# Optimization experiments

Measured on AMD Instinct MI355X. Metric: run time of the kernel, lower is better.

Reference implementation:

```python
import jax, jax.numpy as jnp
import numpy as np

B, T, H = 64, 1024, 256

def _lstm_cell(x, h, c, Wih, Whh, bih, bhh):
    # torch gate order: i, f, g, o
    gates = x @ Wih.T + h @ Whh.T + bih + bhh  # [B, 4H]
    i, f, g, o = jnp.split(gates, 4, axis=-1)
    i = jax.nn.sigmoid(i)
    f = jax.nn.sigmoid(f)
    g = jnp.tanh(g)
    o = jax.nn.sigmoid(o)
    c_new = f * c + i * g
    h_new = o * jnp.tanh(c_new)
    return h_new, c_new


def setup_inputs() -> dict:
    key = jax.random.key(0)
    ks = jax.random.split(key, 11)
    s = 1.0 / np.sqrt(H)
    def u(k, shape):
        return jax.random.uniform(k, shape, jnp.float32, -s, s)
    return {
        "x": jax.random.normal(ks[0], (B, T, 1), jnp.float32),
        "enc_Wih": u(ks[1], (4 * H, 1)),
        "enc_Whh": u(ks[2], (4 * H, H)),
        "enc_bih": u(ks[3], (4 * H,)),
        "enc_bhh": u(ks[4], (4 * H,)),
        "dec_Wih": u(ks[5], (4 * H, 1)),
        "dec_Whh": u(ks[6], (4 * H, H)),
        "dec_bih": u(ks[7], (4 * H,)),
        "dec_bhh": u(ks[8], (4 * H,)),
        "lin_W": u(ks[9], (1, 2 * H)),
        "lin_b": u(ks[10], (1,)),
    }


def reference(x, enc_Wih, enc_Whh, enc_bih, enc_bhh,
              dec_Wih, dec_Whh, dec_bih, dec_bhh, lin_W, lin_b):
    b = x.shape[0]
    h = x.shape[2] * 0  # placeholder, not used
    hidden = enc_Whh.shape[1]

    x_t = jnp.transpose(x, (1, 0, 2))  # [T, B, 1]

    # ---- encoder: single-layer LSTM over time ----
    def enc_step(carry, xt):
        hh, cc = carry
        hh, cc = _lstm_cell(xt, hh, cc, enc_Wih, enc_Whh, enc_bih, enc_bhh)
        return (hh, cc), hh
    h0 = jnp.zeros((b, hidden), x.dtype)
    (h_last, _), enc_seq = jax.lax.scan(enc_step, (h0, h0), x_t)
    encoder_states = jnp.transpose(enc_seq, (1, 0, 2))  # [B, T, H]

    # ---- decoder: LSTMCell + dot attention + linear, per step ----
    def dec_step(carry, xt):
        hx, cx = carry
        hx, cx = _lstm_cell(xt, hx, cx, dec_Wih, dec_Whh, dec_bih, dec_bhh)
        scores = jnp.einsum('bth,bh->bt', encoder_states, hx)  # dot attention
        attn = jax.nn.softmax(scores, axis=1)
        ctx = jnp.einsum('bt,bth->bh', attn, encoder_states)
        updated = jnp.concatenate([ctx, hx], axis=1)  # [B, 2H]
        res = updated @ lin_W.T + lin_b  # [B, 1]
        return (hx, cx), res

    cx0 = jnp.zeros_like(h_last)
    _, outs = jax.lax.scan(dec_step, (h_last, cx0), x_t)  # [T, B, 1]
    return jnp.transpose(outs, (1, 0, 2))  # [B, T, 1]
```

## Files before the change

### kernel.cpp

```cpp
#include <hip/hip_runtime.h>
#include <math.h>

#define HD 256
#define GD 1024
#define TT 1024
#define BB 64
#define NT 512

typedef float __attribute__((ext_vector_type(4))) f32x4;

__device__ __forceinline__ float sig_(float x)  { return 1.f / (1.f + __expf(-x)); }
__device__ __forceinline__ float tanh_(float x) { return 1.f - 2.f / (1.f + __expf(2.f * x)); }

__global__ __launch_bounds__(256) void prep_kernel(
    const float* __restrict__ eW, const float* __restrict__ eb1, const float* __restrict__ eb2,
    const float* __restrict__ dW, const float* __restrict__ db1, const float* __restrict__ db2,
    float* __restrict__ WTe, float* __restrict__ WTd,
    float* __restrict__ be, float* __restrict__ bd,
    unsigned long long* __restrict__ ex,
    unsigned* __restrict__ prog4)
{
    int idx = blockIdx.x * 256 + threadIdx.x;
    if (idx < GD * HD) {
        int j = idx / HD, k = idx % HD;
        WTe[k * GD + j] = eW[idx];
        WTd[k * GD + j] = dW[idx];
    }
    if (idx < GD) {
        be[idx] = eb1[idx] + eb2[idx];
        bd[idx] = db1[idx] + db2[idx];
    }
    if (idx < BB * 2 * 256) ex[idx] = 0ULL;
    if (idx < BB * 4) prog4[idx] = 0u;
}

__device__ __forceinline__ void scan_body(
    const float* __restrict__ x, const float* __restrict__ Wih,
    const float* __restrict__ bias, const float* __restrict__ WT,
    const float* __restrict__ h_init, float* __restrict__ states,
    unsigned long long* __restrict__ ex, unsigned tag0,
    const float* __restrict__ lw, float* __restrict__ qdot,
    unsigned* __restrict__ prog4,
    float* x_s, float* h_rep , float* act_s ,
    int b, int q)
{
    const int tid = threadIdx.x;
    const int s   = tid & 3;
    const int jj  = tid >> 2;
    const int gate = jj >> 5;
    const int kk0  = (jj & 31) * 2;
    const int r0   = gate * 64 + kk0;
    const int jg0  = gate * 256 + q * 64 + kk0;

    float4 w0[16], w1[16];
    {
        const float* basek = WT + (size_t)(s * 64) * GD;
        #pragma unroll
        for (int i = 0; i < 16; ++i) {
            const float* p0 = basek + (size_t)(4 * i) * GD + jg0;
            w0[i] = make_float4(p0[0], p0[GD], p0[2 * GD], p0[3 * GD]);
            const float* p1 = p0 + 1;
            w1[i] = make_float4(p1[0], p1[GD], p1[2 * GD], p1[3 * GD]);
        }
    }
    const float wih0 = Wih[jg0], wih1 = Wih[jg0 + 1];
    const float bj0  = bias[jg0], bj1  = bias[jg0 + 1];
    const float lwd  = lw ? lw[tid & 255] : 0.f;

    for (int i = tid; i < TT; i += NT) x_s[i] = x[b * TT + i];
    if (tid < 256) {
        float hv = h_init ? h_init[((size_t)b * TT + (TT - 1)) * HD + tid] : 0.f;
        h_rep[(tid >> 6) * 264 + (tid & 63)] = hv;
    }
    float c = 0.f;
    __syncthreads();

    #pragma unroll 1
    for (int t = 0; t < TT; ++t) {
        __builtin_amdgcn_s_setprio(1);
        const float xt = x_s[t];
        float a0p, a1p, a0q = 0.f, a1q = 0.f;
        if (s == 0) { a0p = fmaf(xt, wih0, bj0); a1p = fmaf(xt, wih1, bj1); }
        else        { a0p = 0.f;                 a1p = 0.f; }
        const float4* h4 = (const float4*)(h_rep + s * 264);
        #pragma unroll
        for (int i = 0; i < 8; ++i) {
            float4 hv = h4[i];
            a0p = fmaf(hv.x, w0[i].x, a0p); a0p = fmaf(hv.y, w0[i].y, a0p);
            a0p = fmaf(hv.z, w0[i].z, a0p); a0p = fmaf(hv.w, w0[i].w, a0p);
            a1p = fmaf(hv.x, w1[i].x, a1p); a1p = fmaf(hv.y, w1[i].y, a1p);
            a1p = fmaf(hv.z, w1[i].z, a1p); a1p = fmaf(hv.w, w1[i].w, a1p);
        }
        #pragma unroll
        for (int i = 8; i < 16; ++i) {
            float4 hv = h4[i];
            a0q = fmaf(hv.x, w0[i].x, a0q); a0q = fmaf(hv.y, w0[i].y, a0q);
            a0q = fmaf(hv.z, w0[i].z, a0q); a0q = fmaf(hv.w, w0[i].w, a0q);
            a1q = fmaf(hv.x, w1[i].x, a1q); a1q = fmaf(hv.y, w1[i].y, a1q);
            a1q = fmaf(hv.z, w1[i].z, a1q); a1q = fmaf(hv.w, w1[i].w, a1q);
        }
        float a0 = a0p + a0q;
        float a1 = a1p + a1q;
        a0 += __shfl_xor(a0, 1); a0 += __shfl_xor(a0, 2);
        a1 += __shfl_xor(a1, 1); a1 += __shfl_xor(a1, 2);
        if (s == 0) {
            float2 av;
            av.x = (gate == 2) ? tanh_(a0) : sig_(a0);
            av.y = (gate == 2) ? tanh_(a1) : sig_(a1);
            *(float2*)(&act_s[r0]) = av;
        }
        __syncthreads();

        const unsigned tag = tag0 + (unsigned)t + 1u;
        unsigned long long* ssl = ex + ((size_t)b * 2 + (t & 1)) * 256;
        if (tid < 256) {
            const int dq = tid >> 6, dk = tid & 63;
            if (dq == q) {
                float gi = act_s[dk], gf = act_s[64 + dk], gg = act_s[128 + dk], go = act_s[192 + dk];
                c = fmaf(gf, c, gi * gg);
                float h = go * tanh_(c);
                unsigned long long pk = ((unsigned long long)tag << 32)
                                      | (unsigned long long)__float_as_uint(h);
                __hip_atomic_store(&ssl[tid], pk, __ATOMIC_RELAXED, __HIP_MEMORY_SCOPE_AGENT);
                h_rep[q * 264 + dk] = h;
                float* sp = &states[((size_t)(b * TT + t)) * HD + tid];
                asm volatile("global_store_dword %0, %1, off sc0 sc1"
                             :: "v"(sp), "v"(h) : "memory");
                __builtin_amdgcn_s_setprio(0);
                if (lw) {
                    float v = h * lwd;
                    #pragma unroll
                    for (int m = 1; m < 64; m <<= 1) v += __shfl_xor(v, m);
                    if (dk == 0) qdot[((size_t)(b * TT + t)) * 4 + q] = v;
                }
            } else {
                __builtin_amdgcn_s_setprio(0);
                unsigned long long u;
                const unsigned long long* sp = ssl + tid;
                do {
                    u = __hip_atomic_load(sp, __ATOMIC_RELAXED, __HIP_MEMORY_SCOPE_AGENT);
                } while ((unsigned)(u >> 32) != tag);
                h_rep[dq * 264 + dk] = __uint_as_float((unsigned)u);
            }
        } else {
            __builtin_amdgcn_s_setprio(0);
        }
        __syncthreads();
        if (prog4 && ((t & 31) == 31) && tid == 0)
            __hip_atomic_store(&prog4[b * 4 + q], (unsigned)((t + 1) >> 5),
                               __ATOMIC_RELAXED, __HIP_MEMORY_SCOPE_AGENT);
    }
}

__global__ __launch_bounds__(NT, 2) void enc_kernel(
    const float* __restrict__ x, const float* __restrict__ Wih,
    const float* __restrict__ bias, const float* __restrict__ WT,
    float* __restrict__ states, unsigned long long* __restrict__ ex,
    const float* __restrict__ lw, float* __restrict__ qew)
{
    __shared__ float x_s[TT];
    __shared__ float h_rep[4 * 264];
    __shared__ float act_s[256];
    const int b = (int)blockIdx.x & 63;
    const int q = (int)blockIdx.x >> 6;
    scan_body(x, Wih, bias, WT, nullptr, states, ex, 0u, lw, qew, nullptr,
              x_s, h_rep, act_s, b, q);
}

#define SMEMF 17440
__global__ __launch_bounds__(NT, 2) void tail_kernel(
    const float* __restrict__ x, const float* __restrict__ Wih,
    const float* __restrict__ bias, const float* __restrict__ WT,
    const float* __restrict__ enc_states, float* __restrict__ dec_hs,
    unsigned long long* __restrict__ ex,
    unsigned* __restrict__ prog4,
    const float* __restrict__ qew, const float* __restrict__ lw2,
    const float* __restrict__ lin_b, float* __restrict__ out)
{
    __shared__ __align__(16) float smem[SMEMF];
    const int blk = (int)blockIdx.x;
    const int tid = threadIdx.x;

    if (blk < 256) {
        float* x_s   = smem;
        float* h_rep = smem + 1024;
        float* act_s = smem + 1024 + 4 * 264;
        scan_body(x, Wih, bias, WT, enc_states, dec_hs, ex, 1024u,
                  nullptr, nullptr, prog4, x_s, h_rep, act_s, blk & 63, blk >> 6);
        return;
    }

    const int ai   = blk - 256;
    const int b    = ai & 63;
    const int tile = ai >> 6;
    const int td0  = tile * 32;
    float* Hx   = smem;
    float* E    = smem + 9216;
    float* hw_s = smem + 17408;

    if (tid == 0) {
        const unsigned need = (unsigned)tile + 1u;
        for (;;) {
            unsigned m0 = __hip_atomic_load(&prog4[b*4+0], __ATOMIC_RELAXED, __HIP_MEMORY_SCOPE_AGENT);
            unsigned m1 = __hip_atomic_load(&prog4[b*4+1], __ATOMIC_RELAXED, __HIP_MEMORY_SCOPE_AGENT);
            unsigned m2 = __hip_atomic_load(&prog4[b*4+2], __ATOMIC_RELAXED, __HIP_MEMORY_SCOPE_AGENT);
            unsigned m3 = __hip_atomic_load(&prog4[b*4+3], __ATOMIC_RELAXED, __HIP_MEMORY_SCOPE_AGENT);
            unsigned mn = min(min(m0, m1), min(m2, m3));
            if (mn >= need) break;
            __builtin_amdgcn_s_sleep(8);
        }
        (void)__hip_atomic_load(&prog4[b*4], __ATOMIC_ACQUIRE, __HIP_MEMORY_SCOPE_AGENT);
    }
    __syncthreads();

    {
        const int td = tid >> 4;
        const int kq = tid & 15;
        const int kc = kq * 16;
        const float* src = dec_hs + ((size_t)b * TT + td0 + td) * HD + kc;
        f32x4 v0, v1, v2, v3;
        asm volatile(
            "global_load_dwordx4 %0, %4, off sc0 sc1\n\t"
            "global_load_dwordx4 %1, %5, off sc0 sc1\n\t"
            "global_load_dwordx4 %2, %6, off sc0 sc1\n\t"
            "global_load_dwordx4 %3, %7, off sc0 sc1\n\t"
            "s_waitcnt vmcnt(0)"
            : "=&v"(v0), "=&v"(v1), "=&v"(v2), "=&v"(v3)
            : "v"(src), "v"(src + 4), "v"(src + 8), "v"(src + 12)
            : "memory");
        const float4 w20 = ((const float4*)(lw2 + kc))[0];
        const float4 w21 = ((const float4*)(lw2 + kc))[1];
        const float4 w22 = ((const float4*)(lw2 + kc))[2];
        const float4 w23 = ((const float4*)(lw2 + kc))[3];
        float ph = 0.f;
        Hx[(kc+ 0)*36+td]=v0.x; Hx[(kc+ 1)*36+td]=v0.y; Hx[(kc+ 2)*36+td]=v0.z; Hx[(kc+ 3)*36+td]=v0.w;
        Hx[(kc+ 4)*36+td]=v1.x; Hx[(kc+ 5)*36+td]=v1.y; Hx[(kc+ 6)*36+td]=v1.z; Hx[(kc+ 7)*36+td]=v1.w;
        Hx[(kc+ 8)*36+td]=v2.x; Hx[(kc+ 9)*36+td]=v2.y; Hx[(kc+10)*36+td]=v2.z; Hx[(kc+11)*36+td]=v2.w;
        Hx[(kc+12)*36+td]=v3.x; Hx[(kc+13)*36+td]=v3.y; Hx[(kc+14)*36+td]=v3.z; Hx[(kc+15)*36+td]=v3.w;
        ph = fmaf(v0.x, w20.x, ph); ph = fmaf(v0.y, w20.y, ph);
        ph = fmaf(v0.z, w20.z, ph); ph = fmaf(v0.w, w20.w, ph);
        ph = fmaf(v1.x, w21.x, ph); ph = fmaf(v1.y, w21.y, ph);
        ph = fmaf(v1.z, w21.z, ph); ph = fmaf(v1.w, w21.w, ph);
        ph = fmaf(v2.x, w22.x, ph); ph = fmaf(v2.y, w22.y, ph);
        ph = fmaf(v2.z, w22.z, ph); ph = fmaf(v2.w, w22.w, ph);
        ph = fmaf(v3.x, w23.x, ph); ph = fmaf(v3.y, w23.y, ph);
        ph = fmaf(v3.z, w23.z, ph); ph = fmaf(v3.w, w23.w, ph);
        E[td * 16 + kq] = ph;
    }
    __syncthreads();
    if (tid < 32) {
        float sum = 0.f;
        #pragma unroll
        for (int j = 0; j < 16; ++j) sum += E[tid * 16 + j];
        hw_s[tid] = sum;
    }

    const int tdt = tid >> 5;
    const int tet = tid & 31;

    float M[2]  = {-1e30f, -1e30f};
    float Nm[2] = {0.f, 0.f};
    float Dn[2] = {0.f, 0.f};

    for (int tc = 0; tc < 4; ++tc) {
        const int te0 = tc * 256;
        float S[2][8] = {{0.f}};
        for (int kc8 = 0; kc8 < 8; ++kc8) {
            const int k0 = kc8 * 32;
            __syncthreads();
            {
                const int te = tid & 255, half = tid >> 8;
                const float* src = enc_states + ((size_t)b * TT + te0 + te) * HD + k0 + half * 16;
                #pragma unroll
                for (int j = 0; j < 4; ++j) {
                    float4 v = ((const float4*)src)[j];
                    E[(half * 16 + j * 4 + 0) * 256 + te] = v.x;
                    E[(half * 16 + j * 4 + 1) * 256 + te] = v.y;
                    E[(half * 16 + j * 4 + 2) * 256 + te] = v.z;
                    E[(half * 16 + j * 4 + 3) * 256 + te] = v.w;
                }
            }
            __syncthreads();
            #pragma unroll 8
            for (int k = 0; k < 32; ++k) {
                const float2 hx2 = *(const float2*)(&Hx[(k0 + k) * 36 + tdt * 2]);
                #pragma unroll
                for (int i = 0; i < 8; ++i) {
                    const float e = E[k * 256 + tet + 32 * i];
                    S[0][i] = fmaf(hx2.x, e, S[0][i]);
                    S[1][i] = fmaf(hx2.y, e, S[1][i]);
                }
            }
        }
        float ewv[8];
        #pragma unroll
        for (int i = 0; i < 8; ++i) {
            const float4 e4 = ((const float4*)qew)[(size_t)b * TT + te0 + tet + 32 * i];
            ewv[i] = (e4.x + e4.y) + (e4.z + e4.w);
        }
        #pragma unroll
        for (int r = 0; r < 2; ++r) {
            float cm = S[r][0];
            #pragma unroll
            for (int i = 1; i < 8; ++i) cm = fmaxf(cm, S[r][i]);
            #pragma unroll
            for (int m = 1; m < 32; m <<= 1) cm = fmaxf(cm, __shfl_xor(cm, m));
            const float newM  = fmaxf(M[r], cm);
            const float scale = __expf(M[r] - newM);
            float nl = 0.f, dl = 0.f;
            #pragma unroll
            for (int i = 0; i < 8; ++i) {
                const float p = __expf(S[r][i] - newM);
                dl += p;
                nl = fmaf(p, ewv[i], nl);
            }
            #pragma unroll
            for (int m = 1; m < 32; m <<= 1) {
                nl += __shfl_xor(nl, m);
                dl += __shfl_xor(dl, m);
            }
            Nm[r] = Nm[r] * scale + nl;
            Dn[r] = Dn[r] * scale + dl;
            M[r]  = newM;
        }
    }

    if (tet == 0) {
        const float lb = lin_b[0];
        #pragma unroll
        for (int r = 0; r < 2; ++r) {
            const int row = tdt * 2 + r;
            out[(size_t)b * TT + td0 + row] = Nm[r] / Dn[r] + hw_s[row] + lb;
        }
    }
}

extern "C" void kernel_launch(void* const* d_in, const int* in_sizes, int n_in,
                              void* d_out, int out_size, void* d_ws, size_t ws_size,
                              hipStream_t stream)
{
    const float* x    = (const float*)d_in[0];
    const float* eWih = (const float*)d_in[1];
    const float* eWhh = (const float*)d_in[2];
    const float* ebih = (const float*)d_in[3];
    const float* ebhh = (const float*)d_in[4];
    const float* dWih = (const float*)d_in[5];
    const float* dWhh = (const float*)d_in[6];
    const float* dbih = (const float*)d_in[7];
    const float* dbhh = (const float*)d_in[8];
    const float* linW = (const float*)d_in[9];
    const float* linb = (const float*)d_in[10];
    float* out = (float*)d_out;

    float* p = (float*)d_ws;
    float* WTe = p;        p += (size_t)GD * HD;
    float* WTd = p;        p += (size_t)GD * HD;
    float* be  = p;        p += GD;
    float* bd  = p;        p += GD;
    float* enc_states = p; p += (size_t)BB * TT * HD;
    float* dec_hs = p;     p += (size_t)BB * TT * HD;
    float* qew = p;        p += (size_t)BB * TT * 4;
    unsigned long long* ex = (unsigned long long*)p; p += (size_t)BB * 2 * 256 * 2;
    unsigned* prog4 = (unsigned*)p; p += 256;

    prep_kernel<<<(GD * HD + 255) / 256, 256, 0, stream>>>(
        eWhh, ebih, ebhh, dWhh, dbih, dbhh, WTe, WTd, be, bd, ex, prog4);

    enc_kernel<<<256, NT, 0, stream>>>(
        x, eWih, be, WTe, enc_states, ex, linW, qew);

    tail_kernel<<<256 + BB * (TT / 32), NT, 0, stream>>>(
        x, dWih, bd, WTd, enc_states, dec_hs, ex, prog4,
        qew, linW + HD, linb, out);
}
```

Measured before the change: 4.336 ms.

## Double attention tile to 64 decoder rows and compute hx·lin_W inside scan

The attention blocks now each handle 64 decoder timesteps, with 4 rows per thread instead of 2. This halves the number of attention blocks and the number of times each block re-reads the encoder states, at the cost of more registers and shared memory per block. The decoder scan now computes the per-quarter hx·lin_W dot product itself and writes it to a new buffer, so the attention blocks no longer have to compute it. The setprio raise is also hoisted out of the time loop, which keeps the scan blocks at high priority for the whole loop.

Result: faster. 3.997 ms (-7.8%).

```diff
diff --git a/kernel.cpp b/kernel.cpp
--- a/kernel.cpp
+++ b/kernel.cpp
@@ -39,7 +39,7 @@
     const float* __restrict__ bias, const float* __restrict__ WT,
     const float* __restrict__ h_init, float* __restrict__ states,
     unsigned long long* __restrict__ ex, unsigned tag0,
-    const float* __restrict__ lw, float* __restrict__ qdot,
+    const float* __restrict__ lw, float* __restrict__ qdot, int wt,
     unsigned* __restrict__ prog4,
     float* x_s, float* h_rep , float* act_s ,
     int b, int q)
@@ -75,9 +75,9 @@
     float c = 0.f;
     __syncthreads();
 
+    __builtin_amdgcn_s_setprio(1);
     #pragma unroll 1
     for (int t = 0; t < TT; ++t) {
-        __builtin_amdgcn_s_setprio(1);
         const float xt = x_s[t];
         float a0p, a1p, a0q = 0.f, a1q = 0.f;
         if (s == 0) { a0p = fmaf(xt, wih0, bj0); a1p = fmaf(xt, wih1, bj1); }
@@ -126,15 +126,21 @@
                 float* sp = &states[((size_t)(b * TT + t)) * HD + tid];
                 asm volatile("global_store_dword %0, %1, off sc0 sc1"
                              :: "v"(sp), "v"(h) : "memory");
-                __builtin_amdgcn_s_setprio(0);
                 if (lw) {
                     float v = h * lwd;
                     #pragma unroll
                     for (int m = 1; m < 64; m <<= 1) v += __shfl_xor(v, m);
-                    if (dk == 0) qdot[((size_t)(b * TT + t)) * 4 + q] = v;
+                    if (dk == 0) {
+                        float* qp = &qdot[((size_t)(b * TT + t)) * 4 + q];
+                        if (wt) {
+                            asm volatile("global_store_dword %0, %1, off sc0 sc1"
+                                         :: "v"(qp), "v"(v) : "memory");
+                        } else {
+                            *qp = v;
+                        }
+                    }
                 }
             } else {
-                __builtin_amdgcn_s_setprio(0);
                 unsigned long long u;
                 const unsigned long long* sp = ssl + tid;
                 do {
@@ -142,14 +148,13 @@
                 } while ((unsigned)(u >> 32) != tag);
                 h_rep[dq * 264 + dk] = __uint_as_float((unsigned)u);
             }
-        } else {
-            __builtin_amdgcn_s_setprio(0);
         }
         __syncthreads();
         if (prog4 && ((t & 31) == 31) && tid == 0)
             __hip_atomic_store(&prog4[b * 4 + q], (unsigned)((t + 1) >> 5),
                                __ATOMIC_RELAXED, __HIP_MEMORY_SCOPE_AGENT);
     }
+    __builtin_amdgcn_s_setprio(0);
 }
 
 __global__ __launch_bounds__(NT, 2) void enc_kernel(
@@ -163,18 +168,20 @@
     __shared__ float act_s[256];
     const int b = (int)blockIdx.x & 63;
     const int q = (int)blockIdx.x >> 6;
-    scan_body(x, Wih, bias, WT, nullptr, states, ex, 0u, lw, qew, nullptr,
+    scan_body(x, Wih, bias, WT, nullptr, states, ex, 0u, lw, qew, 0, nullptr,
               x_s, h_rep, act_s, b, q);
 }
 
-#define SMEMF 17440
+#define SMEMF 18752
+#define TDA   64
 __global__ __launch_bounds__(NT, 2) void tail_kernel(
     const float* __restrict__ x, const float* __restrict__ Wih,
     const float* __restrict__ bias, const float* __restrict__ WT,
     const float* __restrict__ enc_states, float* __restrict__ dec_hs,
     unsigned long long* __restrict__ ex,
     unsigned* __restrict__ prog4,
-    const float* __restrict__ qew, const float* __restrict__ lw2,
+    const float* __restrict__ qew, float* __restrict__ qhw,
+    const float* __restrict__ lw2,
     const float* __restrict__ lin_b, float* __restrict__ out)
 {
     __shared__ __align__(16) float smem[SMEMF];
@@ -186,20 +193,20 @@
         float* h_rep = smem + 1024;
         float* act_s = smem + 1024 + 4 * 264;
         scan_body(x, Wih, bias, WT, enc_states, dec_hs, ex, 1024u,
-                  nullptr, nullptr, prog4, x_s, h_rep, act_s, blk & 63, blk >> 6);
+                  lw2, qhw, 1, prog4, x_s, h_rep, act_s, blk & 63, blk >> 6);
         return;
     }
 
     const int ai   = blk - 256;
     const int b    = ai & 63;
     const int tile = ai >> 6;
-    const int td0  = tile * 32;
+    const int td0  = tile * TDA;
     float* Hx   = smem;
-    float* E    = smem + 9216;
-    float* hw_s = smem + 17408;
+    float* E    = smem + 64 * 260;
+    float* hw_s = E + 2048;
 
     if (tid == 0) {
-        const unsigned need = (unsigned)tile + 1u;
+        const unsigned need = (unsigned)(tile * 2 + 2);
         for (;;) {
             unsigned m0 = __hip_atomic_load(&prog4[b*4+0], __ATOMIC_RELAXED, __HIP_MEMORY_SCOPE_AGENT);
             unsigned m1 = __hip_atomic_load(&prog4[b*4+1], __ATOMIC_RELAXED, __HIP_MEMORY_SCOPE_AGENT);
@@ -214,81 +221,75 @@
     __syncthreads();
 
     {
-        const int td = tid >> 4;
-        const int kq = tid & 15;
-        const int kc = kq * 16;
-        const float* src = dec_hs + ((size_t)b * TT + td0 + td) * HD + kc;
-        f32x4 v0, v1, v2, v3;
-        asm volatile(
-            "global_load_dwordx4 %0, %4, off sc0 sc1\n\t"
-            "global_load_dwordx4 %1, %5, off sc0 sc1\n\t"
-            "global_load_dwordx4 %2, %6, off sc0 sc1\n\t"
-            "global_load_dwordx4 %3, %7, off sc0 sc1\n\t"
-            "s_waitcnt vmcnt(0)"
-            : "=&v"(v0), "=&v"(v1), "=&v"(v2), "=&v"(v3)
-            : "v"(src), "v"(src + 4), "v"(src + 8), "v"(src + 12)
-            : "memory");
-        const float4 w20 = ((const float4*)(lw2 + kc))[0];
-        const float4 w21 = ((const float4*)(lw2 + kc))[1];
-        const float4 w22 = ((const float4*)(lw2 + kc))[2];
-        const float4 w23 = ((const float4*)(lw2 + kc))[3];
-        float ph = 0.f;
-        Hx[(kc+ 0)*36+td]=v0.x; Hx[(kc+ 1)*36+td]=v0.y; Hx[(kc+ 2)*36+td]=v0.z; Hx[(kc+ 3)*36+td]=v0.w;
-        Hx[(kc+ 4)*36+td]=v1.x; Hx[(kc+ 5)*36+td]=v1.y; Hx[(kc+ 6)*36+td]=v1.z; Hx[(kc+ 7)*36+td]=v1.w;
-        Hx[(kc+ 8)*36+td]=v2.x; Hx[(kc+ 9)*36+td]=v2.y; Hx[(kc+10)*36+td]=v2.z; Hx[(kc+11)*36+td]=v2.w;
-        Hx[(kc+12)*36+td]=v3.x; Hx[(kc+13)*36+td]=v3.y; Hx[(kc+14)*36+td]=v3.z; Hx[(kc+15)*36+td]=v3.w;
-        ph = fmaf(v0.x, w20.x, ph); ph = fmaf(v0.y, w20.y, ph);
-        ph = fmaf(v0.z, w20.z, ph); ph = fmaf(v0.w, w20.w, ph);
-        ph = fmaf(v1.x, w21.x, ph); ph = fmaf(v1.y, w21.y, ph);
-        ph = fmaf(v1.z, w21.z, ph); ph = fmaf(v1.w, w21.w, ph);
-        ph = fmaf(v2.x, w22.x, ph); ph = fmaf(v2.y, w22.y, ph);
-        ph = fmaf(v2.z, w22.z, ph); ph = fmaf(v2.w, w22.w, ph);
-        ph = fmaf(v3.x, w23.x, ph); ph = fmaf(v3.y, w23.y, ph);
-        ph = fmaf(v3.z, w23.z, ph); ph = fmaf(v3.w, w23.w, ph);
-        E[td * 16 + kq] = ph;
-    }
-    __syncthreads();
-    if (tid < 32) {
-        float sum = 0.f;
-        #pragma unroll
-        for (int j = 0; j < 16; ++j) sum += E[tid * 16 + j];
-        hw_s[tid] = sum;
+        const int k   = tid & 255;
+        const int tdg = tid >> 8;
+        #pragma unroll 1
+        for (int j0 = 0; j0 < 32; j0 += 4) {
+            const int tdb = tdg * 32 + j0;
+            const float* s0 = dec_hs + ((size_t)b * TT + td0 + tdb) * HD + k;
+            const float* s1 = s0 + HD;
+            const float* s2 = s0 + 2 * HD;
+            const float* s3 = s0 + 3 * HD;
+            float v0, v1, v2, v3;
+            asm volatile(
+                "global_load_dword %0, %4, off sc0 sc1\n\t"
+                "global_load_dword %1, %5, off sc0 sc1\n\t"
+                "global_load_dword %2, %6, off sc0 sc1\n\t"
+                "global_load_dword %3, %7, off sc0 sc1\n\t"
+                "s_waitcnt vmcnt(0)"
+                : "=&v"(v0), "=&v"(v1), "=&v"(v2), "=&v"(v3)
+                : "v"(s0), "v"(s1), "v"(s2), "v"(s3) : "memory");
+            Hx[(tdb + 0) * 260 + k] = v0;
+            Hx[(tdb + 1) * 260 + k] = v1;
+            Hx[(tdb + 2) * 260 + k] = v2;
+            Hx[(tdb + 3) * 260 + k] = v3;
+        }
+    }
+    if (tid < TDA) {
+        const float* qp = qhw + ((size_t)b * TT + td0 + tid) * 4;
+        f32x4 q4;
+        asm volatile("global_load_dwordx4 %0, %1, off sc0 sc1\n\ts_waitcnt vmcnt(0)"
+                     : "=&v"(q4) : "v"(qp) : "memory");
+        hw_s[tid] = (q4.x + q4.y) + (q4.z + q4.w);
     }
 
     const int tdt = tid >> 5;
     const int tet = tid & 31;
 
-    float M[2]  = {-1e30f, -1e30f};
-    float Nm[2] = {0.f, 0.f};
-    float Dn[2] = {0.f, 0.f};
+    float M[4]  = {-1e30f, -1e30f, -1e30f, -1e30f};
+    float Nm[4] = {0.f, 0.f, 0.f, 0.f};
+    float Dn[4] = {0.f, 0.f, 0.f, 0.f};
 
     for (int tc = 0; tc < 4; ++tc) {
         const int te0 = tc * 256;
-        float S[2][8] = {{0.f}};
-        for (int kc8 = 0; kc8 < 8; ++kc8) {
-            const int k0 = kc8 * 32;
+        float S[4][8] = {{0.f}};
+        for (int kc = 0; kc < 32; ++kc) {
+            const int k0 = kc * 8;
             __syncthreads();
             {
-                const int te = tid & 255, half = tid >> 8;
-                const float* src = enc_states + ((size_t)b * TT + te0 + te) * HD + k0 + half * 16;
-                #pragma unroll
-                for (int j = 0; j < 4; ++j) {
-                    float4 v = ((const float4*)src)[j];
-                    E[(half * 16 + j * 4 + 0) * 256 + te] = v.x;
-                    E[(half * 16 + j * 4 + 1) * 256 + te] = v.y;
-                    E[(half * 16 + j * 4 + 2) * 256 + te] = v.z;
-                    E[(half * 16 + j * 4 + 3) * 256 + te] = v.w;
-                }
+                const int te = tid & 255, kg = tid >> 8;
+                const float* src = enc_states + ((size_t)b * TT + te0 + te) * HD + k0 + kg * 4;
+                float4 v = *(const float4*)src;
+                E[(kg * 4 + 0) * 256 + te] = v.x;
+                E[(kg * 4 + 1) * 256 + te] = v.y;
+                E[(kg * 4 + 2) * 256 + te] = v.z;
+                E[(kg * 4 + 3) * 256 + te] = v.w;
             }
             __syncthreads();
-            #pragma unroll 8
-            for (int k = 0; k < 32; ++k) {
-                const float2 hx2 = *(const float2*)(&Hx[(k0 + k) * 36 + tdt * 2]);
+            #pragma unroll
+            for (int k = 0; k < 8; ++k) {
+                const int kk = k0 + k;
+                const float hx0 = Hx[(tdt * 4 + 0) * 260 + kk];
+                const float hx1 = Hx[(tdt * 4 + 1) * 260 + kk];
+                const float hx2 = Hx[(tdt * 4 + 2) * 260 + kk];
+                const float hx3 = Hx[(tdt * 4 + 3) * 260 + kk];
                 #pragma unroll
                 for (int i = 0; i < 8; ++i) {
                     const float e = E[k * 256 + tet + 32 * i];
-                    S[0][i] = fmaf(hx2.x, e, S[0][i]);
-                    S[1][i] = fmaf(hx2.y, e, S[1][i]);
+                    S[0][i] = fmaf(hx0, e, S[0][i]);
+                    S[1][i] = fmaf(hx1, e, S[1][i]);
+                    S[2][i] = fmaf(hx2, e, S[2][i]);
+                    S[3][i] = fmaf(hx3, e, S[3][i]);
                 }
             }
         }
@@ -299,7 +300,7 @@
             ewv[i] = (e4.x + e4.y) + (e4.z + e4.w);
         }
         #pragma unroll
-        for (int r = 0; r < 2; ++r) {
+        for (int r = 0; r < 4; ++r) {
             float cm = S[r][0];
             #pragma unroll
             for (int i = 1; i < 8; ++i) cm = fmaxf(cm, S[r][i]);
@@ -328,8 +329,8 @@
     if (tet == 0) {
         const float lb = lin_b[0];
         #pragma unroll
-        for (int r = 0; r < 2; ++r) {
-            const int row = tdt * 2 + r;
+        for (int r = 0; r < 4; ++r) {
+            const int row = tdt * 4 + r;
             out[(size_t)b * TT + td0 + row] = Nm[r] / Dn[r] + hw_s[row] + lb;
         }
     }
@@ -360,6 +361,7 @@
     float* enc_states = p; p += (size_t)BB * TT * HD;
     float* dec_hs = p;     p += (size_t)BB * TT * HD;
     float* qew = p;        p += (size_t)BB * TT * 4;
+    float* qhw = p;        p += (size_t)BB * TT * 4;
     unsigned long long* ex = (unsigned long long*)p; p += (size_t)BB * 2 * 256 * 2;
     unsigned* prog4 = (unsigned*)p; p += 256;
 
@@ -369,7 +371,7 @@
     enc_kernel<<<256, NT, 0, stream>>>(
         x, eWih, be, WTe, enc_states, ex, linW, qew);
 
-    tail_kernel<<<256 + BB * (TT / 32), NT, 0, stream>>>(
+    tail_kernel<<<256 + BB * (TT / TDA), NT, 0, stream>>>(
         x, dWih, bd, WTd, enc_states, dec_hs, ex, prog4,
-        qew, linW + HD, linb, out);
-}
+        qew, qhw, linW + HD, linb, out);
+}
```
